# Kernel tuning notes

Measured on AMD Instinct MI355X. Metric: run time of the kernel, lower is better.

The kernel has to match this reference:

```python
import jax, jax.numpy as jnp
import numpy as np

D_MODEL = 2048
N_HEADS = 16
D_K = D_MODEL // N_HEADS
D_FF = 8192
EPS = 1e-5


def layer_norm(x, gamma, beta):
    mu = jnp.mean(x, axis=-1, keepdims=True)
    var = jnp.var(x, axis=-1, keepdims=True)
    return (x - mu) * jax.lax.rsqrt(var + EPS) * gamma + beta


def setup_inputs() -> dict:
    key = jax.random.key(0)
    ks = jax.random.split(key, 10)
    B, S = 2, 2048
    x = jax.random.normal(ks[0], (B, S, D_MODEL), dtype=jnp.float32)
    mask = jnp.ones((1, 1, S, S), dtype=jnp.int32)  # all-visible (masked_fill where mask==0)
    sc = 0.02
    w_qkv = jax.random.normal(ks[1], (D_MODEL, 3 * D_MODEL), dtype=jnp.float32) * sc
    w_o = jax.random.normal(ks[2], (D_MODEL, D_MODEL), dtype=jnp.float32) * sc
    gamma1 = jnp.ones((D_MODEL,), jnp.float32)
    beta1 = jnp.zeros((D_MODEL,), jnp.float32)
    gamma2 = jnp.ones((D_MODEL,), jnp.float32)
    beta2 = jnp.zeros((D_MODEL,), jnp.float32)
    w1 = jax.random.normal(ks[3], (D_MODEL, D_FF), dtype=jnp.float32) * sc
    b1 = jnp.zeros((D_FF,), jnp.float32)
    w2 = jax.random.normal(ks[4], (D_FF, D_MODEL), dtype=jnp.float32) * sc
    b2 = jnp.zeros((D_MODEL,), jnp.float32)
    layer_scale = jnp.full((1, 1, D_MODEL), 0.1, jnp.float32)
    return {"x": x, "mask": mask, "w_qkv": w_qkv, "w_o": w_o,
            "gamma1": gamma1, "beta1": beta1, "gamma2": gamma2, "beta2": beta2,
            "w1": w1, "b1": b1, "w2": w2, "b2": b2, "layer_scale": layer_scale}


def reference(x, mask, w_qkv, w_o, gamma1, beta1, gamma2, beta2, w1, b1, w2, b2, layer_scale):
    B, S, _ = x.shape
    # parallel residual: both norms applied to x
    attn_in = layer_norm(x, gamma1, beta1)
    ff_in = layer_norm(x, gamma2, beta2)

    # --- attention (dropout = identity in eval) ---
    qkv = attn_in @ w_qkv                          # [B,S,3D]
    q, k, v = jnp.split(qkv, 3, axis=-1)
    def heads(t):
        return t.reshape(B, S, N_HEADS, D_K).transpose(0, 2, 1, 3)  # [B,H,S,dk]
    q, k, v = heads(q), heads(k), heads(v)
    scores = jnp.einsum('bhqd,bhkd->bhqk', q, k) / np.sqrt(D_K).astype(np.float32)
    scores = jnp.where(mask == 0, jnp.float32(-1e9), scores)
    probs = jax.nn.softmax(scores, axis=-1)
    ctx = jnp.einsum('bhqk,bhkd->bhqd', probs, v)
    ctx = ctx.transpose(0, 2, 1, 3).reshape(B, S, D_MODEL)
    attn_out = ctx @ w_o

    # --- feed forward with layer scale ---
    h = jax.nn.gelu(ff_in @ w1 + b1, approximate=False)
    ff_out = layer_scale * (h @ w2 + b2)

    return x + attn_out + ff_out
```

## Files before the change

### kernel.cpp

```cpp
#include <hip/hip_runtime.h>
#include <math.h>

#define TOK 4096
#define DM 2048
#define SL 2048
#define NHEAD 16
#define DKH 128
#define DFF 8192

typedef float f32x4 __attribute__((ext_vector_type(4)));
typedef __bf16 bf16x8 __attribute__((ext_vector_type(8)));
typedef unsigned short u16x8 __attribute__((ext_vector_type(8)));

__device__ __forceinline__ unsigned short f2bf(float f) {
  unsigned int u = __float_as_uint(f);
  u += 0x7fffu + ((u >> 16) & 1u);
  return (unsigned short)(u >> 16);
}
__device__ __forceinline__ float bf2f(unsigned short h) {
  return __uint_as_float((unsigned int)h << 16);
}

__device__ __forceinline__ void gload_lds16(const void* g, void* l) {
  __builtin_amdgcn_global_load_lds(
      (const __attribute__((address_space(1))) unsigned int*)g,
      (__attribute__((address_space(3))) unsigned int*)l, 16, 0, 0);
}

__global__ __launch_bounds__(256) void ln_cast_kernel(
    const float* __restrict__ x, const float* __restrict__ g1,
    const float* __restrict__ be1, const float* __restrict__ g2,
    const float* __restrict__ be2, unsigned short* __restrict__ attn_in,
    unsigned short* __restrict__ ff_in) {
  __shared__ float redS[4], redQ[4];
  long row = blockIdx.x;
  int t = threadIdx.x;
  const float4* xr = (const float4*)(x + row * DM);
  float4 a = xr[t];
  float4 b = xr[t + 256];
  float s = a.x + a.y + a.z + a.w + b.x + b.y + b.z + b.w;
  float q = a.x * a.x + a.y * a.y + a.z * a.z + a.w * a.w +
            b.x * b.x + b.y * b.y + b.z * b.z + b.w * b.w;
  for (int o = 32; o > 0; o >>= 1) {
    s += __shfl_xor(s, o, 64);
    q += __shfl_xor(q, o, 64);
  }
  int wave = t >> 6;
  if ((t & 63) == 0) { redS[wave] = s; redQ[wave] = q; }
  __syncthreads();
  s = redS[0] + redS[1] + redS[2] + redS[3];
  q = redQ[0] + redQ[1] + redQ[2] + redQ[3];
  float mean = s * (1.0f / DM);
  float var = q * (1.0f / DM) - mean * mean;
  float rs = rsqrtf(var + 1e-5f);
  float vals[8] = {a.x, a.y, a.z, a.w, b.x, b.y, b.z, b.w};
  long base = row * DM;
#pragma unroll
  for (int i = 0; i < 8; ++i) {
    int c = (i < 4) ? (4 * t + i) : (1024 + 4 * t + (i - 4));
    float nv = (vals[i] - mean) * rs;
    attn_in[base + c] = f2bf(nv * g1[c] + be1[c]);
    ff_in[base + c] = f2bf(nv * g2[c] + be2[c]);
  }
}

__global__ __launch_bounds__(256) void transpose_cast(
    const float* __restrict__ in, unsigned short* __restrict__ out, int R, int C) {
  __shared__ float tile[32][33];
  int bx = blockIdx.x << 5;
  int by = blockIdx.y << 5;
  int tx = threadIdx.x & 31, ty = threadIdx.x >> 5;
#pragma unroll
  for (int i = ty; i < 32; i += 8) tile[i][tx] = in[(long)(by + i) * C + bx + tx];
  __syncthreads();
#pragma unroll
  for (int i = ty; i < 32; i += 8)
    out[(long)(bx + i) * R + by + tx] = f2bf(tile[tx][i]);
}

__global__ __launch_bounds__(256) void transpose_v(
    const unsigned short* __restrict__ qkv, unsigned short* __restrict__ v_t) {
  __shared__ unsigned short tile[32][33];
  int z = blockIdx.z;
  int b = z >> 4, h = z & 15;
  int sx = blockIdx.x << 5;
  int dx = blockIdx.y << 5;
  int tx = threadIdx.x & 31, ty = threadIdx.x >> 5;
  const unsigned short* src = qkv + (long)b * SL * (3 * DM) + 2 * DM + h * DKH;
#pragma unroll
  for (int i = ty; i < 32; i += 8)
    tile[i][tx] = src[(long)(sx + i) * (3 * DM) + dx + tx];
  __syncthreads();
  unsigned short* dst = v_t + (long)z * DKH * SL;
#pragma unroll
  for (int i = ty; i < 32; i += 8)
    dst[(long)(dx + i) * SL + sx + tx] = tile[tx][i];
}

__global__ __launch_bounds__(256) void softmax_bf16(unsigned short* __restrict__ sc) {
  __shared__ float red[4];
  long row = blockIdx.x;
  unsigned short* rp = sc + row * (long)SL;
  int t = threadIdx.x, wave = t >> 6;
  u16x8 u = ((const u16x8*)rp)[t];
  const float scale = 0.08838834764831845f;
  float v[8];
  float mx = -1e30f;
#pragma unroll
  for (int i = 0; i < 8; ++i) { v[i] = bf2f(u[i]) * scale; mx = fmaxf(mx, v[i]); }
  for (int o = 32; o > 0; o >>= 1) mx = fmaxf(mx, __shfl_xor(mx, o, 64));
  if ((t & 63) == 0) red[wave] = mx;
  __syncthreads();
  mx = fmaxf(fmaxf(red[0], red[1]), fmaxf(red[2], red[3]));
  __syncthreads();
  float sum = 0.f;
#pragma unroll
  for (int i = 0; i < 8; ++i) { v[i] = __expf(v[i] - mx); sum += v[i]; }
  for (int o = 32; o > 0; o >>= 1) sum += __shfl_xor(sum, o, 64);
  if ((t & 63) == 0) red[wave] = sum;
  __syncthreads();
  float inv = 1.0f / (red[0] + red[1] + red[2] + red[3]);
  u16x8 o;
#pragma unroll
  for (int i = 0; i < 8; ++i) o[i] = f2bf(v[i] * inv);
  ((u16x8*)rp)[t] = o;
}

__global__ __launch_bounds__(256) void combine_ctx(unsigned short* __restrict__ c0,
                                                   const unsigned short* __restrict__ c1) {
  long i = (long)blockIdx.x * 256 + threadIdx.x;
  u16x8 a = ((const u16x8*)c0)[i];
  u16x8 b = ((const u16x8*)c1)[i];
  u16x8 o;
#pragma unroll
  for (int j = 0; j < 8; ++j) o[j] = f2bf(bf2f(a[j]) + bf2f(b[j]));
  ((u16x8*)c0)[i] = o;
}

__global__ __launch_bounds__(256) void combine_wo(const float* __restrict__ x,
                                                  const unsigned short* __restrict__ p0,
                                                  const unsigned short* __restrict__ p1,
                                                  float* __restrict__ out) {
  long i = ((long)blockIdx.x * 256 + threadIdx.x) * 8;
  u16x8 a = *(const u16x8*)(p0 + i);
  u16x8 b = *(const u16x8*)(p1 + i);
#pragma unroll
  for (int j = 0; j < 8; ++j) out[i + j] = x[i + j] + bf2f(a[j]) + bf2f(b[j]);
}

__global__ __launch_bounds__(256) void combine_ff(const unsigned short* __restrict__ p0,
                                                  const unsigned short* __restrict__ p1,
                                                  const float* __restrict__ ls,
                                                  const float* __restrict__ b2,
                                                  float* __restrict__ out) {
  long i = ((long)blockIdx.x * 256 + threadIdx.x) * 8;
  u16x8 a = *(const u16x8*)(p0 + i);
  u16x8 b = *(const u16x8*)(p1 + i);
#pragma unroll
  for (int j = 0; j < 8; ++j) {
    int col = (int)((i + j) & (DM - 1));
    out[i + j] += ls[col] * (bf2f(a[j]) + bf2f(b[j]) + b2[col]);
  }
}

struct GemmP {
  const unsigned short* A;
  const unsigned short* B;
  const float* bias;
  const float* xadd;
  const float* lscale;
  float* outf;
  unsigned short* outb;
  int K;
  int lda, ldb, ldc;
  long sAz, sAo, sAi;
  long sBz, sBo, sBi;
  long sCz, sCo, sCi;
  long sKz;
  int innerN, zbase, nksplit;
};

template <int EPI>
__global__ __launch_bounds__(256, 2) void gemm_bt(GemmP p) {
  __shared__ __align__(16) unsigned short As[128 * 32];
  __shared__ __align__(16) unsigned short Bs[128 * 32];
  const int tid = threadIdx.x;
  const int wave = tid >> 6;
  const int lane = tid & 63;
  const int quad = lane >> 4;
  const int l16 = lane & 15;
  const int wm = (wave >> 1) << 6;
  const int wn = (wave & 1) << 6;
  const long m0 = (long)blockIdx.y << 7;
  const long n0 = (long)blockIdx.x << 7;
  const int kz = blockIdx.z % p.nksplit;
  const int zlog = blockIdx.z / p.nksplit;
  const int zz = p.zbase + zlog;
  const int zq = zz / p.innerN;
  const int zr = zz - zq * p.innerN;
  const long koff = (long)kz * p.K;
  const unsigned short* Ab =
      p.A + (long)zlog * p.sAz + (long)zq * p.sAo + (long)zr * p.sAi + koff;
  const unsigned short* Bb =
      p.B + (long)zlog * p.sBz + (long)zq * p.sBo + (long)zr * p.sBi + koff;
  const long offC =
      (long)zlog * p.sCz + (long)zq * p.sCo + (long)zr * p.sCi + (long)kz * p.sKz;

  f32x4 acc[4][4];
#pragma unroll
  for (int i = 0; i < 4; ++i)
#pragma unroll
    for (int j = 0; j < 4; ++j)
#pragma unroll
      for (int r = 0; r < 4; ++r) acc[i][j][r] = 0.0f;

  const int r0 = tid >> 2;
  const int r1 = r0 + 64;
  const int csw = (((tid & 3) ^ ((r0 >> 1) & 3)) << 3);
  unsigned short* lA0 = As + (long)(tid & ~63) * 8;
  unsigned short* lA1 = As + (long)(256 + (tid & ~63)) * 8;
  unsigned short* lB0 = Bs + (long)(tid & ~63) * 8;
  unsigned short* lB1 = Bs + (long)(256 + (tid & ~63)) * 8;

  for (int k0 = 0; k0 < p.K; k0 += 32) {
    gload_lds16(Ab + (m0 + r0) * (long)p.lda + k0 + csw, lA0);
    gload_lds16(Ab + (m0 + r1) * (long)p.lda + k0 + csw, lA1);
    gload_lds16(Bb + (n0 + r0) * (long)p.ldb + k0 + csw, lB0);
    gload_lds16(Bb + (n0 + r1) * (long)p.ldb + k0 + csw, lB1);
    __syncthreads();
    bf16x8 af[4], bf[4];
#pragma unroll
    for (int i = 0; i < 4; ++i) {
      int rA = wm + i * 16 + l16;
      af[i] = *(const bf16x8*)(As + (((rA << 2) + (quad ^ ((rA >> 1) & 3))) << 3));
      int rB = wn + i * 16 + l16;
      bf[i] = *(const bf16x8*)(Bs + (((rB << 2) + (quad ^ ((rB >> 1) & 3))) << 3));
    }
#pragma unroll
    for (int i = 0; i < 4; ++i)
#pragma unroll
      for (int j = 0; j < 4; ++j)
        acc[i][j] =
            __builtin_amdgcn_mfma_f32_16x16x32_bf16(af[i], bf[j], acc[i][j], 0, 0, 0);
    __syncthreads();
  }

#pragma unroll
  for (int i = 0; i < 4; ++i)
#pragma unroll
    for (int j = 0; j < 4; ++j)
#pragma unroll
      for (int r = 0; r < 4; ++r) {
        long m = m0 + wm + i * 16 + quad * 4 + r;
        long n = n0 + wn + j * 16 + l16;
        long idx = offC + m * (long)p.ldc + n;
        float v = acc[i][j][r];
        if (EPI == 0) {
          p.outb[idx] = f2bf(v);
        } else if (EPI == 2) {
          float u = v + p.bias[n];
          p.outb[idx] = f2bf(0.5f * u * (1.0f + erff(u * 0.70710678118654752f)));
        } else if (EPI == 3) {
          p.outf[idx] = p.xadd[m * (long)p.ldc + n] + v;
        } else {
          p.outf[idx] += p.lscale[n] * (v + p.bias[n]);
        }
      }
}

template <int EPI>
__global__ __launch_bounds__(512, 2) void gemm256(GemmP p) {
  __shared__ __align__(16) unsigned short As[2 * 2 * 8192];
  __shared__ __align__(16) unsigned short Bs[2 * 2 * 8192];
  const int tid = threadIdx.x;
  const int wavu = __builtin_amdgcn_readfirstlane(tid >> 6);
  const int lane = tid & 63;
  const int quad = lane >> 4;
  const int l16 = lane & 15;
  const int wm = (wavu >> 2) << 7;
  const int wn = (wavu & 3) << 6;

  const int nwg = gridDim.x * gridDim.y;
  const int orig = blockIdx.y * gridDim.x + blockIdx.x;
  int sw = orig;
  if ((nwg & 7) == 0) sw = (orig & 7) * (nwg >> 3) + (orig >> 3);
  const int bx = sw % gridDim.x;
  const int by = sw / gridDim.x;
  const long m0 = (long)by << 8;
  const long n0 = (long)bx << 8;

  const int kz = blockIdx.z % p.nksplit;
  const int zlog = blockIdx.z / p.nksplit;
  const int zz = p.zbase + zlog;
  const int zq = zz / p.innerN;
  const int zr = zz - zq * p.innerN;
  const long koff = (long)kz * p.K;
  const unsigned short* Ab =
      p.A + (long)zlog * p.sAz + (long)zq * p.sAo + (long)zr * p.sAi + koff;
  const unsigned short* Bb =
      p.B + (long)zlog * p.sBz + (long)zq * p.sBo + (long)zr * p.sBi + koff;
  const long offC =
      (long)zlog * p.sCz + (long)zq * p.sCo + (long)zr * p.sCi + (long)kz * p.sKz;
  const int NT = p.K >> 6;

  f32x4 acc[8][4];
#pragma unroll
  for (int i = 0; i < 8; ++i)
#pragma unroll
    for (int j = 0; j < 4; ++j)
#pragma unroll
      for (int r = 0; r < 4; ++r) acc[i][j][r] = 0.0f;

  bf16x8 afr[4][2];
  bf16x8 bfr[4][2];

  const unsigned short* pA[2][2];
  const unsigned short* pB[2][2];
#pragma unroll
  for (int l = 0; l < 2; ++l) {
    const int rr = (wavu << 4) + (l << 3) + (lane >> 3);
    const int gcb = (lane & 7) ^ (rr & 7);
#pragma unroll
    for (int mh = 0; mh < 2; ++mh) {
      const long growA = m0 + (long)(((rr >> 6) << 7) + (mh << 6) + (rr & 63));
      pA[mh][l] = Ab + growA * (long)p.lda + (gcb << 3);
    }
#pragma unroll
    for (int nh = 0; nh < 2; ++nh) {
      const long growB = n0 + (long)(((rr >> 5) << 6) + (nh << 5) + (rr & 31));
      pB[nh][l] = Bb + growB * (long)p.ldb + (gcb << 3);
    }
  }

  int aoffA[2], boffB[2];
#pragma unroll
  for (int ks = 0; ks < 2; ++ks) {
    const int swz = (((ks << 2) | quad) ^ (l16 & 7)) << 4;
    aoffA[ks] = ((wavu >> 2) << 13) + (l16 << 7) + swz;
    boffB[ks] = ((wavu & 3) << 12) + (l16 << 7) + swz;
  }
  const char* const AsB = (const char*)As;
  const char* const BsB = (const char*)Bs;
  unsigned short* const dA0 = As + (wavu << 10);
  unsigned short* const dB0 = Bs + (wavu << 10);

#define BAR() __builtin_amdgcn_s_barrier()
#define VMW(n) asm volatile("s_waitcnt vmcnt(" #n ")" ::: "memory")

#define STAGE_A(buf, mh, off)                                                     \
  do {                                                                            \
    _Pragma("unroll") for (int l = 0; l < 2; ++l)                                 \
        gload_lds16(pA[mh][l] + (off),                                            \
                    dA0 + (((buf) << 14) + ((mh) << 13)) + (l << 9));             \
  } while (0)

#define STAGE_B(buf, nh, off)                                                     \
  do {                                                                            \
    _Pragma("unroll") for (int l = 0; l < 2; ++l)                                 \
        gload_lds16(pB[nh][l] + (off),                                            \
                    dB0 + (((buf) << 14) + ((nh) << 13)) + (l << 9));             \
  } while (0)

#define LOAD_AF(buf, mh)                                                          \
  do {                                                                            \
    _Pragma("unroll") for (int i = 0; i < 4; ++i)                                 \
        _Pragma("unroll") for (int ks = 0; ks < 2; ++ks)                          \
            afr[i][ks] = *(const bf16x8*)(AsB + aoffA[ks] +                       \
                                          (((buf) << 15) + ((mh) << 14) +         \
                                           (i << 11)));                           \
  } while (0)

#define LOAD_BF(buf, nh)                                                          \
  do {                                                                            \
    _Pragma("unroll") for (int j = 0; j < 2; ++j)                                 \
        _Pragma("unroll") for (int ks = 0; ks < 2; ++ks)                          \
            bfr[(nh) * 2 + j][ks] = *(const bf16x8*)(BsB + boffB[ks] +            \
                                                     (((buf) << 15) +             \
                                                      ((nh) << 14) +              \
                                                      (j << 11)));                \
  } while (0)

#define MMA_QUAD(mh, nh)                                                          \
  do {                                                                            \
    __builtin_amdgcn_s_setprio(1);                                                \
    _Pragma("unroll") for (int i = 0; i < 4; ++i)                                 \
        _Pragma("unroll") for (int j = 0; j < 2; ++j)                             \
            _Pragma("unroll") for (int ks = 0; ks < 2; ++ks)                      \
                acc[(mh) * 4 + i][(nh) * 2 + j] =                                 \
                    __builtin_amdgcn_mfma_f32_16x16x32_bf16(                      \
                        afr[i][ks], bfr[(nh) * 2 + j][ks],                        \
                        acc[(mh) * 4 + i][(nh) * 2 + j], 0, 0, 0);                \
    __builtin_amdgcn_s_setprio(0);                                                \
  } while (0)

#define KSTEP(BUF, OFF1, OFF2, S1, S2, VMQ)                                       \
  do {                                                                            \
    LOAD_AF(BUF, 0);                                                              \
    LOAD_BF(BUF, 0);                                                              \
    if (S1) STAGE_A((BUF) ^ 1, 1, OFF1);                                          \
    BAR();                                                                        \
    MMA_QUAD(0, 0);                                                               \
    BAR();                                                                        \
    LOAD_BF(BUF, 1);                                                              \
    if (S1) STAGE_B((BUF) ^ 1, 1, OFF1);                                          \
    BAR();                                                                        \
    MMA_QUAD(0, 1);                                                               \
    BAR();                                                                        \
    LOAD_AF(BUF, 1);                                                              \
    if (S2) STAGE_A(BUF, 0, OFF2);                                                \
    BAR();                                                                        \
    MMA_QUAD(1, 0);                                                               \
    BAR();                                                                        \
    if (S2) STAGE_B(BUF, 0, OFF2);                                                \
    BAR();                                                                        \
    MMA_QUAD(1, 1);                                                               \
    VMQ;                                                                          \
    BAR();                                                                        \
  } while (0)

  STAGE_A(0, 0, 0);
  STAGE_B(0, 0, 0);
  STAGE_A(0, 1, 0);
  STAGE_B(0, 1, 0);
  STAGE_A(1, 0, 64);
  STAGE_B(1, 0, 64);
  VMW(4);
  BAR();
#pragma unroll
  for (int l = 0; l < 2; ++l) {
    pA[0][l] += 64; pA[1][l] += 64; pB[0][l] += 64; pB[1][l] += 64;
  }

  const int half = NT >> 1;
#pragma unroll 1
  for (int u = 0; u + 1 < half; ++u) {
    KSTEP(0, 0, 64, true, true, VMW(4));
    KSTEP(1, 64, 128, true, true, VMW(4));
#pragma unroll
    for (int l = 0; l < 2; ++l) {
      pA[0][l] += 128; pA[1][l] += 128; pB[0][l] += 128; pB[1][l] += 128;
    }
  }
  KSTEP(0, 0, 0, true, false, VMW(0));
  KSTEP(1, 0, 0, false, false, ((void)0));

#undef KSTEP
#undef MMA_QUAD
#undef LOAD_BF
#undef LOAD_AF
#undef STAGE_B
#undef STAGE_A
#undef VMW
#undef BAR

#pragma unroll
  for (int I = 0; I < 8; ++I)
#pragma unroll
    for (int J = 0; J < 4; ++J)
#pragma unroll
      for (int r = 0; r < 4; ++r) {
        long m = m0 + wm + I * 16 + quad * 4 + r;
        long n = n0 + wn + J * 16 + l16;
        long idx = offC + m * (long)p.ldc + n;
        float v = acc[I][J][r];
        if (EPI == 0) {
          p.outb[idx] = f2bf(v);
        } else if (EPI == 2) {
          float u = v + p.bias[n];
          p.outb[idx] = f2bf(0.5f * u * (1.0f + erff(u * 0.70710678118654752f)));
        } else if (EPI == 3) {
          p.outf[idx] = p.xadd[m * (long)p.ldc + n] + v;
        } else {
          p.outf[idx] += p.lscale[n] * (v + p.bias[n]);
        }
      }
}

extern "C" void kernel_launch(void* const* d_in, const int* in_sizes, int n_in,
                              void* d_out, int out_size, void* d_ws, size_t ws_size,
                              hipStream_t stream) {
  const float* x = (const float*)d_in[0];
  const float* w_qkv = (const float*)d_in[2];
  const float* w_o = (const float*)d_in[3];
  const float* g1 = (const float*)d_in[4];
  const float* be1 = (const float*)d_in[5];
  const float* g2 = (const float*)d_in[6];
  const float* be2 = (const float*)d_in[7];
  const float* w1 = (const float*)d_in[8];
  const float* b1 = (const float*)d_in[9];
  const float* w2 = (const float*)d_in[10];
  const float* b2 = (const float*)d_in[11];
  const float* ls = (const float*)d_in[12];
  float* out = (float*)d_out;

  unsigned char* ws = (unsigned char*)d_ws;
  const size_t MiB = 1024 * 1024;
  unsigned short* qkv = (unsigned short*)(ws);
  unsigned short* v_t = (unsigned short*)(ws + 48 * MiB);
  unsigned short* ff_in = (unsigned short*)(ws + 64 * MiB);
  unsigned short* attn_in = (unsigned short*)(ws + 80 * MiB);
  unsigned short* ctxC0 = (unsigned short*)(ws + 80 * MiB);
  unsigned short* ctxC1 = (unsigned short*)(ws + 96 * MiB);
  unsigned short* wbuf = (unsigned short*)(ws + 96 * MiB);
  unsigned short* h1 = (unsigned short*)(ws);
  unsigned short* scores = (unsigned short*)(ws + 128 * MiB);
  unsigned short* P0 = (unsigned short*)(ws + 128 * MiB);
  unsigned short* P1 = (unsigned short*)(ws + 144 * MiB);

  int chunk;
  bool split;
  if (ws_size >= 264 * MiB)      { chunk = 16; split = true; }
  else if (ws_size >= 196 * MiB) { chunk = 8;  split = true; }
  else if (ws_size >= 162 * MiB) { chunk = 4;  split = true; }
  else                           { chunk = 2;  split = false; }

  const long ODM = (long)TOK * DM;
  dim3 blk(256);
  dim3 blk512(512);

  ln_cast_kernel<<<TOK, blk, 0, stream>>>(x, g1, be1, g2, be2, attn_in, ff_in);

  {
    transpose_cast<<<dim3(3 * DM / 32, DM / 32), blk, 0, stream>>>(w_qkv, wbuf, DM, 3 * DM);
    GemmP p = {};
    p.A = attn_in; p.B = wbuf; p.outb = qkv;
    p.K = DM; p.lda = DM; p.ldb = DM; p.ldc = 3 * DM;
    p.innerN = 1; p.nksplit = 1;
    gemm256<0><<<dim3(3 * DM / 256, TOK / 256, 1), blk512, 0, stream>>>(p);
  }

  transpose_v<<<dim3(SL / 32, DKH / 32, 32), blk, 0, stream>>>(qkv, v_t);

  for (int c0 = 0; c0 < 32; c0 += chunk) {
    {
      GemmP p = {};
      p.A = qkv; p.B = qkv + DM; p.outb = scores;
      p.K = DKH; p.lda = 3 * DM; p.ldb = 3 * DM; p.ldc = SL;
      p.sAo = (long)SL * 3 * DM; p.sAi = DKH;
      p.sBo = (long)SL * 3 * DM; p.sBi = DKH;
      p.sCz = (long)SL * SL;
      p.innerN = NHEAD; p.zbase = c0; p.nksplit = 1;
      gemm_bt<0><<<dim3(SL / 128, SL / 128, chunk), blk, 0, stream>>>(p);
    }
    softmax_bf16<<<chunk * SL, blk, 0, stream>>>(scores);
    {
      GemmP p = {};
      p.A = scores; p.B = v_t; p.outb = ctxC0;
      p.K = split ? SL / 2 : SL; p.lda = SL; p.ldb = SL; p.ldc = DM;
      p.sAz = (long)SL * SL;
      p.sBo = (long)NHEAD * DKH * SL; p.sBi = (long)DKH * SL;
      p.sCo = (long)SL * DM; p.sCi = DKH;
      p.sKz = ODM;
      p.innerN = NHEAD; p.zbase = c0; p.nksplit = split ? 2 : 1;
      gemm_bt<0><<<dim3(DKH / 128, SL / 128, chunk * p.nksplit), blk, 0, stream>>>(p);
    }
  }
  if (split)
    combine_ctx<<<(int)(ODM / 2048), blk, 0, stream>>>(ctxC0, ctxC1);

  {
    transpose_cast<<<dim3(DM / 32, DM / 32), blk, 0, stream>>>(w_o, wbuf, DM, DM);
    GemmP p = {};
    p.A = ctxC0; p.B = wbuf;
    p.K = split ? DM / 2 : DM; p.lda = DM; p.ldb = DM; p.ldc = DM;
    p.sKz = ODM; p.innerN = 1; p.nksplit = split ? 2 : 1;
    if (split) {
      p.outb = P0;
      gemm256<0><<<dim3(DM / 256, TOK / 256, 2), blk512, 0, stream>>>(p);
      combine_wo<<<(int)(ODM / 2048), blk, 0, stream>>>(x, P0, P1, out);
    } else {
      p.outf = out; p.xadd = x;
      gemm256<3><<<dim3(DM / 256, TOK / 256, 1), blk512, 0, stream>>>(p);
    }
  }
  {
    transpose_cast<<<dim3(DFF / 32, DM / 32), blk, 0, stream>>>(w1, wbuf, DM, DFF);
    GemmP p = {};
    p.A = ff_in; p.B = wbuf; p.outb = h1; p.bias = b1;
    p.K = DM; p.lda = DM; p.ldb = DM; p.ldc = DFF;
    p.innerN = 1; p.nksplit = 1;
    gemm256<2><<<dim3(DFF / 256, TOK / 256, 1), blk512, 0, stream>>>(p);
  }
  {
    transpose_cast<<<dim3(DM / 32, DFF / 32), blk, 0, stream>>>(w2, wbuf, DFF, DM);
    GemmP p = {};
    p.A = h1; p.B = wbuf;
    p.K = split ? DFF / 2 : DFF; p.lda = DFF; p.ldb = DFF; p.ldc = DM;
    p.sKz = ODM; p.innerN = 1; p.nksplit = split ? 2 : 1;
    if (split) {
      p.outb = P0;
      gemm256<0><<<dim3(DM / 256, TOK / 256, 2), blk512, 0, stream>>>(p);
      combine_ff<<<(int)(ODM / 2048), blk, 0, stream>>>(P0, P1, ls, b2, out);
    } else {
      p.outf = out; p.bias = b2; p.lscale = ls;
      gemm256<4><<<dim3(DM / 256, TOK / 256, 1), blk512, 0, stream>>>(p);
    }
  }
}
```

Before: 1.049 ms.

## Replace materialized QK^T/softmax/PV attention with fused flash-attention kernel

Replaces the chunked pipeline (scores GEMM, row softmax, split-K PV GEMM plus combine) with a single flash-attention kernel. It uses online softmax, double-buffered K/V tiles loaded straight into LDS, and P staged through LDS for the PV MFMA. This removes writing and reading the full 2048x2048 bf16 score matrices, the extra launches and the ctx combine step. The grid has only 512 blocks of 512 threads with heavy register use, so occupancy and the serial per-block loop over 32 KV tiles could limit throughput.

After: 899.1 us. 1.17x faster.

```diff
diff --git a/kernel.cpp b/kernel.cpp
--- a/kernel.cpp
+++ b/kernel.cpp
@@ -97,46 +97,6 @@
     dst[(long)(dx + i) * SL + sx + tx] = tile[tx][i];
 }
 
-__global__ __launch_bounds__(256) void softmax_bf16(unsigned short* __restrict__ sc) {
-  __shared__ float red[4];
-  long row = blockIdx.x;
-  unsigned short* rp = sc + row * (long)SL;
-  int t = threadIdx.x, wave = t >> 6;
-  u16x8 u = ((const u16x8*)rp)[t];
-  const float scale = 0.08838834764831845f;
-  float v[8];
-  float mx = -1e30f;
-#pragma unroll
-  for (int i = 0; i < 8; ++i) { v[i] = bf2f(u[i]) * scale; mx = fmaxf(mx, v[i]); }
-  for (int o = 32; o > 0; o >>= 1) mx = fmaxf(mx, __shfl_xor(mx, o, 64));
-  if ((t & 63) == 0) red[wave] = mx;
-  __syncthreads();
-  mx = fmaxf(fmaxf(red[0], red[1]), fmaxf(red[2], red[3]));
-  __syncthreads();
-  float sum = 0.f;
-#pragma unroll
-  for (int i = 0; i < 8; ++i) { v[i] = __expf(v[i] - mx); sum += v[i]; }
-  for (int o = 32; o > 0; o >>= 1) sum += __shfl_xor(sum, o, 64);
-  if ((t & 63) == 0) red[wave] = sum;
-  __syncthreads();
-  float inv = 1.0f / (red[0] + red[1] + red[2] + red[3]);
-  u16x8 o;
-#pragma unroll
-  for (int i = 0; i < 8; ++i) o[i] = f2bf(v[i] * inv);
-  ((u16x8*)rp)[t] = o;
-}
-
-__global__ __launch_bounds__(256) void combine_ctx(unsigned short* __restrict__ c0,
-                                                   const unsigned short* __restrict__ c1) {
-  long i = (long)blockIdx.x * 256 + threadIdx.x;
-  u16x8 a = ((const u16x8*)c0)[i];
-  u16x8 b = ((const u16x8*)c1)[i];
-  u16x8 o;
-#pragma unroll
-  for (int j = 0; j < 8; ++j) o[j] = f2bf(bf2f(a[j]) + bf2f(b[j]));
-  ((u16x8*)c0)[i] = o;
-}
-
 __global__ __launch_bounds__(256) void combine_wo(const float* __restrict__ x,
                                                   const unsigned short* __restrict__ p0,
                                                   const unsigned short* __restrict__ p1,
@@ -180,92 +140,159 @@
   int innerN, zbase, nksplit;
 };
 
-template <int EPI>
-__global__ __launch_bounds__(256, 2) void gemm_bt(GemmP p) {
-  __shared__ __align__(16) unsigned short As[128 * 32];
-  __shared__ __align__(16) unsigned short Bs[128 * 32];
+__global__ __launch_bounds__(512) void flash_attn(
+    const unsigned short* __restrict__ qkv, const unsigned short* __restrict__ v_t,
+    unsigned short* __restrict__ ctx) {
+  __shared__ __align__(16) unsigned short Ks[2 * 8192];
+  __shared__ __align__(16) unsigned short Vs[2 * 8192];
+  __shared__ __align__(16) unsigned short Pl[8 * 1152];
   const int tid = threadIdx.x;
-  const int wave = tid >> 6;
-  const int lane = tid & 63;
-  const int quad = lane >> 4;
-  const int l16 = lane & 15;
-  const int wm = (wave >> 1) << 6;
-  const int wn = (wave & 1) << 6;
-  const long m0 = (long)blockIdx.y << 7;
-  const long n0 = (long)blockIdx.x << 7;
-  const int kz = blockIdx.z % p.nksplit;
-  const int zlog = blockIdx.z / p.nksplit;
-  const int zz = p.zbase + zlog;
-  const int zq = zz / p.innerN;
-  const int zr = zz - zq * p.innerN;
-  const long koff = (long)kz * p.K;
-  const unsigned short* Ab =
-      p.A + (long)zlog * p.sAz + (long)zq * p.sAo + (long)zr * p.sAi + koff;
-  const unsigned short* Bb =
-      p.B + (long)zlog * p.sBz + (long)zq * p.sBo + (long)zr * p.sBi + koff;
-  const long offC =
-      (long)zlog * p.sCz + (long)zq * p.sCo + (long)zr * p.sCi + (long)kz * p.sKz;
-
-  f32x4 acc[4][4];
-#pragma unroll
-  for (int i = 0; i < 4; ++i)
-#pragma unroll
-    for (int j = 0; j < 4; ++j)
-#pragma unroll
-      for (int r = 0; r < 4; ++r) acc[i][j][r] = 0.0f;
-
-  const int r0 = tid >> 2;
-  const int r1 = r0 + 64;
-  const int csw = (((tid & 3) ^ ((r0 >> 1) & 3)) << 3);
-  unsigned short* lA0 = As + (long)(tid & ~63) * 8;
-  unsigned short* lA1 = As + (long)(256 + (tid & ~63)) * 8;
-  unsigned short* lB0 = Bs + (long)(tid & ~63) * 8;
-  unsigned short* lB1 = Bs + (long)(256 + (tid & ~63)) * 8;
-
-  for (int k0 = 0; k0 < p.K; k0 += 32) {
-    gload_lds16(Ab + (m0 + r0) * (long)p.lda + k0 + csw, lA0);
-    gload_lds16(Ab + (m0 + r1) * (long)p.lda + k0 + csw, lA1);
-    gload_lds16(Bb + (n0 + r0) * (long)p.ldb + k0 + csw, lB0);
-    gload_lds16(Bb + (n0 + r1) * (long)p.ldb + k0 + csw, lB1);
-    __syncthreads();
-    bf16x8 af[4], bf[4];
-#pragma unroll
-    for (int i = 0; i < 4; ++i) {
-      int rA = wm + i * 16 + l16;
-      af[i] = *(const bf16x8*)(As + (((rA << 2) + (quad ^ ((rA >> 1) & 3))) << 3));
-      int rB = wn + i * 16 + l16;
-      bf[i] = *(const bf16x8*)(Bs + (((rB << 2) + (quad ^ ((rB >> 1) & 3))) << 3));
-    }
-#pragma unroll
-    for (int i = 0; i < 4; ++i)
-#pragma unroll
-      for (int j = 0; j < 4; ++j)
-        acc[i][j] =
-            __builtin_amdgcn_mfma_f32_16x16x32_bf16(af[i], bf[j], acc[i][j], 0, 0, 0);
-    __syncthreads();
-  }
-
-#pragma unroll
-  for (int i = 0; i < 4; ++i)
-#pragma unroll
-    for (int j = 0; j < 4; ++j)
-#pragma unroll
-      for (int r = 0; r < 4; ++r) {
-        long m = m0 + wm + i * 16 + quad * 4 + r;
-        long n = n0 + wn + j * 16 + l16;
-        long idx = offC + m * (long)p.ldc + n;
-        float v = acc[i][j][r];
-        if (EPI == 0) {
-          p.outb[idx] = f2bf(v);
-        } else if (EPI == 2) {
-          float u = v + p.bias[n];
-          p.outb[idx] = f2bf(0.5f * u * (1.0f + erff(u * 0.70710678118654752f)));
-        } else if (EPI == 3) {
-          p.outf[idx] = p.xadd[m * (long)p.ldc + n] + v;
-        } else {
-          p.outf[idx] += p.lscale[n] * (v + p.bias[n]);
-        }
-      }
+  const int wave = tid >> 6, lane = tid & 63, quad = lane >> 4, l16 = lane & 15;
+  const int orig = blockIdx.y * gridDim.x + blockIdx.x;
+  const int sw = (orig & 7) * 64 + (orig >> 3);
+  const int qt = sw & 15, bh = sw >> 4;
+  const int b = bh >> 4, h = bh & 15;
+  const long qrow0 = (long)b * SL + qt * 128;
+  const unsigned short* qb = qkv + qrow0 * (3 * DM) + h * DKH;
+  const unsigned short* kb = qkv + ((long)b * SL) * (3 * DM) + DM + h * DKH;
+  const unsigned short* vb = v_t + (long)bh * DKH * SL;
+
+  bf16x8 aq[4];
+#pragma unroll
+  for (int kf = 0; kf < 4; ++kf)
+    aq[kf] =
+        *(const bf16x8*)(qb + (long)(wave * 16 + l16) * (3 * DM) + kf * 32 + quad * 8);
+
+  f32x4 o[8];
+#pragma unroll
+  for (int d = 0; d < 8; ++d)
+#pragma unroll
+    for (int r = 0; r < 4; ++r) o[d][r] = 0.f;
+  float m_[4] = {-1e30f, -1e30f, -1e30f, -1e30f};
+  float l_[4] = {0.f, 0.f, 0.f, 0.f};
+
+  const unsigned short* kp[2];
+  const unsigned short* vp[2];
+#pragma unroll
+  for (int i = 0; i < 2; ++i) {
+    const int f = tid + i * 512;
+    {
+      const int kf = f >> 8, g = f & 255, r = g >> 2, c = g & 3;
+      kp[i] = kb + (long)r * (3 * DM) + kf * 32 + ((c ^ ((r >> 1) & 3)) << 3);
+    }
+    {
+      const int kvf = f >> 9, g = f & 511, r = g >> 2, c = g & 3;
+      vp[i] = vb + (long)r * SL + kvf * 32 + ((c ^ ((r >> 1) & 3)) << 3);
+    }
+  }
+  unsigned short* const kd = Ks + tid * 8;
+  unsigned short* const vd = Vs + tid * 8;
+
+#define FVMW(n) asm volatile("s_waitcnt vmcnt(" #n ")" ::: "memory")
+#define FBAR() __builtin_amdgcn_s_barrier()
+#define FSTAGE(buf)                                                              \
+  do {                                                                           \
+    _Pragma("unroll") for (int i = 0; i < 2; ++i) {                              \
+      gload_lds16(kp[i], kd + (buf) * 8192 + i * 4096);                          \
+      gload_lds16(vp[i], vd + (buf) * 8192 + i * 4096);                          \
+      kp[i] += 64 * 3 * DM;                                                      \
+      vp[i] += 64;                                                               \
+    }                                                                            \
+  } while (0)
+
+#define FBODY(CUR, DOSTAGE)                                                      \
+  do {                                                                           \
+    if (DOSTAGE) {                                                               \
+      FSTAGE((CUR) ^ 1);                                                         \
+      FVMW(4);                                                                   \
+    } else {                                                                     \
+      FVMW(0);                                                                   \
+    }                                                                            \
+    FBAR();                                                                      \
+    f32x4 s[4];                                                                  \
+    _Pragma("unroll") for (int j = 0; j < 4; ++j)                                \
+        _Pragma("unroll") for (int r = 0; r < 4; ++r) s[j][r] = 0.f;             \
+    __builtin_amdgcn_s_setprio(1);                                               \
+    _Pragma("unroll") for (int kf = 0; kf < 4; ++kf) {                           \
+      _Pragma("unroll") for (int j = 0; j < 4; ++j) {                            \
+        const int rB = 16 * j + l16;                                             \
+        bf16x8 bk = *(const bf16x8*)(Ks + (CUR) * 8192 + kf * 2048 +             \
+                                     (((rB << 2) + (quad ^ ((rB >> 1) & 3)))     \
+                                      << 3));                                    \
+        s[j] = __builtin_amdgcn_mfma_f32_16x16x32_bf16(aq[kf], bk, s[j], 0, 0,   \
+                                                       0);                       \
+      }                                                                          \
+    }                                                                            \
+    __builtin_amdgcn_s_setprio(0);                                               \
+    float tmax[4] = {-1e30f, -1e30f, -1e30f, -1e30f};                            \
+    _Pragma("unroll") for (int j = 0; j < 4; ++j)                                \
+        _Pragma("unroll") for (int r = 0; r < 4; ++r) {                          \
+      s[j][r] *= 0.08838834764831845f;                                           \
+      tmax[r] = fmaxf(tmax[r], s[j][r]);                                         \
+    }                                                                            \
+    _Pragma("unroll") for (int r = 0; r < 4; ++r) {                              \
+      _Pragma("unroll") for (int d = 1; d <= 8; d <<= 1)                         \
+          tmax[r] = fmaxf(tmax[r], __shfl_xor(tmax[r], d, 64));                  \
+      const float mn = fmaxf(m_[r], tmax[r]);                                    \
+      const float scl = __expf(m_[r] - mn);                                      \
+      m_[r] = mn;                                                                \
+      l_[r] *= scl;                                                              \
+      _Pragma("unroll") for (int d = 0; d < 8; ++d) o[d][r] *= scl;              \
+    }                                                                            \
+    float rs_[4] = {0.f, 0.f, 0.f, 0.f};                                         \
+    _Pragma("unroll") for (int j = 0; j < 4; ++j)                                \
+        _Pragma("unroll") for (int r = 0; r < 4; ++r) {                          \
+      const float pv = __expf(s[j][r] - m_[r]);                                  \
+      s[j][r] = pv;                                                              \
+      rs_[r] += pv;                                                              \
+    }                                                                            \
+    _Pragma("unroll") for (int r = 0; r < 4; ++r) {                              \
+      _Pragma("unroll") for (int d = 1; d <= 8; d <<= 1)                         \
+          rs_[r] += __shfl_xor(rs_[r], d, 64);                                   \
+      l_[r] += rs_[r];                                                           \
+    }                                                                            \
+    _Pragma("unroll") for (int j = 0; j < 4; ++j)                                \
+        _Pragma("unroll") for (int r = 0; r < 4; ++r)                            \
+            Pl[wave * 1152 + (quad * 4 + r) * 72 + l16 + 16 * j] =               \
+                f2bf(s[j][r]);                                                   \
+    bf16x8 ap0 = *(const bf16x8*)(Pl + wave * 1152 + l16 * 72 + quad * 8);       \
+    bf16x8 ap1 = *(const bf16x8*)(Pl + wave * 1152 + l16 * 72 + 32 + quad * 8);  \
+    __builtin_amdgcn_s_setprio(1);                                               \
+    _Pragma("unroll") for (int df = 0; df < 8; ++df) {                           \
+      const int rV = 16 * df + l16;                                              \
+      const int vsw = (((rV << 2) + (quad ^ ((rV >> 1) & 3))) << 3);             \
+      bf16x8 bv0 = *(const bf16x8*)(Vs + (CUR) * 8192 + vsw);                    \
+      o[df] = __builtin_amdgcn_mfma_f32_16x16x32_bf16(ap0, bv0, o[df], 0, 0, 0); \
+      bf16x8 bv1 = *(const bf16x8*)(Vs + (CUR) * 8192 + 4096 + vsw);             \
+      o[df] = __builtin_amdgcn_mfma_f32_16x16x32_bf16(ap1, bv1, o[df], 0, 0, 0); \
+    }                                                                            \
+    __builtin_amdgcn_s_setprio(0);                                               \
+    FBAR();                                                                      \
+  } while (0)
+
+  FSTAGE(0);
+#pragma unroll 1
+  for (int t2 = 0; t2 < 15; ++t2) {
+    FBODY(0, true);
+    FBODY(1, true);
+  }
+  FBODY(0, true);
+  FBODY(1, false);
+
+#undef FBODY
+#undef FSTAGE
+#undef FBAR
+#undef FVMW
+
+  float inv[4];
+#pragma unroll
+  for (int r = 0; r < 4; ++r) inv[r] = 1.0f / l_[r];
+  unsigned short* cb = ctx + (qrow0 + wave * 16) * DM + h * DKH;
+#pragma unroll
+  for (int df = 0; df < 8; ++df)
+#pragma unroll
+    for (int r = 0; r < 4; ++r)
+      cb[(long)(quad * 4 + r) * DM + l16 + 16 * df] = f2bf(o[df][r] * inv[r]);
 }
 
 template <int EPI>
@@ -500,19 +527,12 @@
   unsigned short* ff_in = (unsigned short*)(ws + 64 * MiB);
   unsigned short* attn_in = (unsigned short*)(ws + 80 * MiB);
   unsigned short* ctxC0 = (unsigned short*)(ws + 80 * MiB);
-  unsigned short* ctxC1 = (unsigned short*)(ws + 96 * MiB);
   unsigned short* wbuf = (unsigned short*)(ws + 96 * MiB);
   unsigned short* h1 = (unsigned short*)(ws);
-  unsigned short* scores = (unsigned short*)(ws + 128 * MiB);
   unsigned short* P0 = (unsigned short*)(ws + 128 * MiB);
   unsigned short* P1 = (unsigned short*)(ws + 144 * MiB);
 
-  int chunk;
-  bool split;
-  if (ws_size >= 264 * MiB)      { chunk = 16; split = true; }
-  else if (ws_size >= 196 * MiB) { chunk = 8;  split = true; }
-  else if (ws_size >= 162 * MiB) { chunk = 4;  split = true; }
-  else                           { chunk = 2;  split = false; }
+  const bool split = ws_size >= 162 * MiB;
 
   const long ODM = (long)TOK * DM;
   dim3 blk(256);
@@ -531,32 +551,7 @@
 
   transpose_v<<<dim3(SL / 32, DKH / 32, 32), blk, 0, stream>>>(qkv, v_t);
 
-  for (int c0 = 0; c0 < 32; c0 += chunk) {
-    {
-      GemmP p = {};
-      p.A = qkv; p.B = qkv + DM; p.outb = scores;
-      p.K = DKH; p.lda = 3 * DM; p.ldb = 3 * DM; p.ldc = SL;
-      p.sAo = (long)SL * 3 * DM; p.sAi = DKH;
-      p.sBo = (long)SL * 3 * DM; p.sBi = DKH;
-      p.sCz = (long)SL * SL;
-      p.innerN = NHEAD; p.zbase = c0; p.nksplit = 1;
-      gemm_bt<0><<<dim3(SL / 128, SL / 128, chunk), blk, 0, stream>>>(p);
-    }
-    softmax_bf16<<<chunk * SL, blk, 0, stream>>>(scores);
-    {
-      GemmP p = {};
-      p.A = scores; p.B = v_t; p.outb = ctxC0;
-      p.K = split ? SL / 2 : SL; p.lda = SL; p.ldb = SL; p.ldc = DM;
-      p.sAz = (long)SL * SL;
-      p.sBo = (long)NHEAD * DKH * SL; p.sBi = (long)DKH * SL;
-      p.sCo = (long)SL * DM; p.sCi = DKH;
-      p.sKz = ODM;
-      p.innerN = NHEAD; p.zbase = c0; p.nksplit = split ? 2 : 1;
-      gemm_bt<0><<<dim3(DKH / 128, SL / 128, chunk * p.nksplit), blk, 0, stream>>>(p);
-    }
-  }
-  if (split)
-    combine_ctx<<<(int)(ODM / 2048), blk, 0, stream>>>(ctxC0, ctxC1);
+  flash_attn<<<dim3(16, 32), blk512, 0, stream>>>(qkv, v_t, ctxC0);
 
   {
     transpose_cast<<<dim3(DM / 32, DM / 32), blk, 0, stream>>>(w_o, wbuf, DM, DM);
```
